# Kernel optimization log

Measured on AMD Instinct MI355X. Metric: run time of the kernel, lower is better.

## Reference

```python
import jax, jax.numpy as jnp
import numpy as np

L, H, D, A, T = 2, 8, 512, 64, 256  # layers, heads, model_dim, attention_dim, target_dim
B, S = 2, 2048
EPS = 1e-5


def _ln(x, g, b):
    m = jnp.mean(x, axis=-1, keepdims=True)
    v = jnp.mean((x - m) ** 2, axis=-1, keepdims=True)
    return (x - m) / jnp.sqrt(v + EPS) * g + b


def setup_inputs() -> dict:
    key = jax.random.key(0)
    ks = jax.random.split(key, 16)
    s = 0.02
    inp = {
        "x": jax.random.normal(ks[0], (B, S, D), jnp.float32),
        # per-head QKV projections, stacked over layers and heads
        "Wq": jax.random.normal(ks[1], (L, H, D, A), jnp.float32) * s,
        "bq": jnp.zeros((L, H, A), jnp.float32),
        "Wk": jax.random.normal(ks[2], (L, H, D, A), jnp.float32) * s,
        "bk": jnp.zeros((L, H, A), jnp.float32),
        "Wv": jax.random.normal(ks[3], (L, H, D, A), jnp.float32) * s,
        "bv": jnp.zeros((L, H, A), jnp.float32),
        # output projection of concatenated heads: [H*A, D]
        "Wo": jax.random.normal(ks[4], (L, H * A, D), jnp.float32) * s,
        "bo": jnp.zeros((L, D), jnp.float32),
        # AddNorm after attention
        "ln1_g": jnp.ones((L, D), jnp.float32),
        "ln1_b": jnp.zeros((L, D), jnp.float32),
        # FFN (hidden_dim == model_dim in this module)
        "W1": jax.random.normal(ks[5], (L, D, D), jnp.float32) * s,
        "b1": jnp.zeros((L, D), jnp.float32),
        "W2": jax.random.normal(ks[6], (L, D, D), jnp.float32) * s,
        "b2": jnp.zeros((L, D), jnp.float32),
        # AddNorm after FFN
        "ln2_g": jnp.ones((L, D), jnp.float32),
        "ln2_b": jnp.zeros((L, D), jnp.float32),
        # final projection to target_dim
        "Wp": jax.random.normal(ks[7], (D, T), jnp.float32) * s,
        "bp": jnp.zeros((T,), jnp.float32),
    }
    return inp


def reference(x, Wq, bq, Wk, bk, Wv, bv, Wo, bo, ln1_g, ln1_b,
              W1, b1, W2, b2, ln2_g, ln2_b, Wp, bp):
    scale = 1.0 / jnp.sqrt(jnp.asarray(A, x.dtype))
    for i in range(L):
        # batched per-head QKV projections (math identical to per-head Linears)
        q = jnp.einsum('bsd,hda->bhsa', x, Wq[i]) + bq[i][:, None, :]
        k = jnp.einsum('bsd,hda->bhsa', x, Wk[i]) + bk[i][:, None, :]
        v = jnp.einsum('bsd,hda->bhsa', x, Wv[i]) + bv[i][:, None, :]
        scores = jnp.einsum('bhsa,bhta->bhst', q, k) * scale  # [B,H,S,S]
        attn = jax.nn.softmax(scores, axis=-1)
        heads = jnp.einsum('bhst,bhta->bhsa', attn, v)        # [B,H,S,A]
        concat = heads.transpose(0, 2, 1, 3).reshape(x.shape[0], x.shape[1], H * A)
        mha = concat @ Wo[i] + bo[i]
        x = _ln(x + mha, ln1_g[i], ln1_b[i])
        ffn = jax.nn.relu(x @ W1[i] + b1[i]) @ W2[i] + b2[i]
        x = _ln(x + ffn, ln2_g[i], ln2_b[i])
    return x @ Wp + bp
```

## Files before the change

kernel.cpp:

```cpp
#include <hip/hip_runtime.h>
#include <hip/hip_bf16.h>

#define MDIM 4096
#define DDIM 512
#define ADIM 64
#define HHEADS 8
#define SLEN 2048
#define TDIM 256
#define SPLIT 4

typedef __attribute__((ext_vector_type(8))) short short8;
typedef __attribute__((ext_vector_type(16))) float f32x16;

__device__ __forceinline__ unsigned short f2bf(float f) {
    union { __hip_bfloat16 h; unsigned short u; } c;
    c.h = __float2bfloat16(f);
    return c.u;
}
__device__ __forceinline__ float bf2f(short s) {
    return __uint_as_float((unsigned)(unsigned short)s << 16);
}

#define N1 524288
#define N2 524288
#define NP 131072
__global__ __launch_bounds__(256) void prep_k(
    const float* __restrict__ Wq, const float* __restrict__ Wk, const float* __restrict__ Wv,
    const float* __restrict__ Wo, const float* __restrict__ W1, const float* __restrict__ W2,
    const float* __restrict__ Wp, const float* __restrict__ x,
    short* __restrict__ Wqt, short* __restrict__ Wkt, short* __restrict__ Wvt,
    short* __restrict__ Wot, short* __restrict__ W1t, short* __restrict__ W2t,
    short* __restrict__ Wpt, short* __restrict__ xbf)
{
    long idx = (long)blockIdx.x * 256 + threadIdx.x;
    if (idx < 3L * N1) {
        int t = (int)(idx / N1);
        int r = (int)(idx % N1);
        int a = r & 63, k = (r >> 6) & 511, hh = r >> 15;
        const float* src = (t == 0) ? Wq : (t == 1) ? Wk : Wv;
        short* dst = (t == 0) ? Wqt : (t == 1) ? Wkt : Wvt;
        dst[((size_t)hh << 15) + (a << 9) + k] = (short)f2bf(src[r]);
        return;
    }
    idx -= 3L * N1;
    if (idx < 3L * N2) {
        int t = (int)(idx / N2);
        int r = (int)(idx % N2);
        int n = r & 511, k = (r >> 9) & 511, i = r >> 18;
        const float* src = (t == 0) ? Wo : (t == 1) ? W1 : W2;
        short* dst = (t == 0) ? Wot : (t == 1) ? W1t : W2t;
        dst[((size_t)i << 18) + (n << 9) + k] = (short)f2bf(src[r]);
        return;
    }
    idx -= 3L * N2;
    if (idx < NP) {
        int r = (int)idx;
        int n = r & 255, k = r >> 8;
        Wpt[n * 512 + k] = (short)f2bf(Wp[r]);
        return;
    }
    idx -= NP;
    xbf[idx] = (short)f2bf(x[idx]);
}

#define LDT 66
__global__ __launch_bounds__(256, 2) void gemm_bf(
    const short* __restrict__ A, const short* __restrict__ Bt,
    const float* __restrict__ bias, void* __restrict__ Cout,
    int M, int N, int K, int flags)
{
    __shared__ short As[64 * LDT];
    __shared__ short Bs[64 * LDT];
    const int tid = threadIdx.x;
    const int wave = tid >> 6, lane = tid & 63;
    const int l31 = lane & 31, hi = lane >> 5;
    const int wm = wave >> 1, wn = wave & 1;
    const int m0 = blockIdx.y * 64, n0 = blockIdx.x * 64;

    f32x16 acc;
#pragma unroll
    for (int r = 0; r < 16; ++r) acc[r] = 0.f;

    const int sr = tid >> 2;
    const int sc = (tid & 3) * 16;

    for (int k0 = 0; k0 < K; k0 += 64) {
        __syncthreads();
        *(short8*)&As[sr * LDT + sc]     = *(const short8*)&A[(size_t)(m0 + sr) * K + k0 + sc];
        *(short8*)&As[sr * LDT + sc + 8] = *(const short8*)&A[(size_t)(m0 + sr) * K + k0 + sc + 8];
        *(short8*)&Bs[sr * LDT + sc]     = *(const short8*)&Bt[(size_t)(n0 + sr) * K + k0 + sc];
        *(short8*)&Bs[sr * LDT + sc + 8] = *(const short8*)&Bt[(size_t)(n0 + sr) * K + k0 + sc + 8];
        __syncthreads();

        short8 af[4], bfm[4];
#pragma unroll
        for (int ks = 0; ks < 4; ++ks) {
            af[ks]  = *(const short8*)&As[(wm * 32 + l31) * LDT + ks * 16 + hi * 8];
            bfm[ks] = *(const short8*)&Bs[(wn * 32 + l31) * LDT + ks * 16 + hi * 8];
        }
#pragma unroll
        for (int ks = 0; ks < 4; ++ks)
            acc = __builtin_amdgcn_mfma_f32_32x32x16_bf16(af[ks], bfm[ks], acc, 0, 0, 0);
    }

    const int col = n0 + wn * 32 + l31;
    const float bb = bias[col];
    const int rbase = m0 + wm * 32 + 4 * hi;
#pragma unroll
    for (int r = 0; r < 16; ++r) {
        int row = rbase + (r & 3) + 8 * (r >> 2);
        float v = acc[r] + bb;
        if (flags & 1) v = fmaxf(v, 0.f);
        if (flags & 2) ((short*)Cout)[(size_t)row * N + col] = (short)f2bf(v);
        else           ((float*)Cout)[(size_t)row * N + col] = v;
    }
}

#define EXPC 0.1803368801111244f

__global__ __launch_bounds__(256, 2) void qkv_bf(
    const short* __restrict__ A,
    const short* __restrict__ Wqt, const short* __restrict__ Wkt, const short* __restrict__ Wvt,
    const float* __restrict__ bq, const float* __restrict__ bk, const float* __restrict__ bv,
    short* __restrict__ Oq, short* __restrict__ Ok, short* __restrict__ Ov)
{
    __shared__ short As[128 * LDT];
    __shared__ short Bs[64 * LDT];
    const int tid = threadIdx.x;
    const int wave = tid >> 6, lane = tid & 63;
    const int l31 = lane & 31, hi = lane >> 5;
    const int wm = wave >> 1, wn = wave & 1;
    const int m0 = blockIdx.y * 128;
    const int nt = blockIdx.x;
    const int which = nt >> 3, h = nt & 7;

    const short* Bt = ((which == 0) ? Wqt : (which == 1) ? Wkt : Wvt) + (size_t)h * 64 * 512;
    const float* bias = ((which == 0) ? bq : (which == 1) ? bk : bv) + h * 64;
    short* Out = (which == 0) ? Oq : (which == 1) ? Ok : Ov;

    f32x16 acc[2];
#pragma unroll
    for (int ms = 0; ms < 2; ++ms)
#pragma unroll
        for (int r = 0; r < 16; ++r) acc[ms][r] = 0.f;

    const int sr = tid >> 3;
    const int sc = (tid & 7) * 8;

    for (int k0 = 0; k0 < 512; k0 += 64) {
        __syncthreads();
#pragma unroll
        for (int p = 0; p < 4; ++p)
            *(short8*)&As[(p * 32 + sr) * LDT + sc] =
                *(const short8*)&A[(size_t)(m0 + p * 32 + sr) * 512 + k0 + sc];
#pragma unroll
        for (int p = 0; p < 2; ++p)
            *(short8*)&Bs[(p * 32 + sr) * LDT + sc] =
                *(const short8*)&Bt[(size_t)(p * 32 + sr) * 512 + k0 + sc];
        __syncthreads();

        short8 af[2][4], bfm[4];
#pragma unroll
        for (int ms = 0; ms < 2; ++ms)
#pragma unroll
            for (int ks = 0; ks < 4; ++ks)
                af[ms][ks] = *(const short8*)&As[(wm * 64 + ms * 32 + l31) * LDT + ks * 16 + hi * 8];
#pragma unroll
        for (int ks = 0; ks < 4; ++ks)
            bfm[ks] = *(const short8*)&Bs[(wn * 32 + l31) * LDT + ks * 16 + hi * 8];
#pragma unroll
        for (int ms = 0; ms < 2; ++ms)
#pragma unroll
            for (int ks = 0; ks < 4; ++ks)
                acc[ms] = __builtin_amdgcn_mfma_f32_32x32x16_bf16(af[ms][ks], bfm[ks], acc[ms], 0, 0, 0);
    }

    const int a = wn * 32 + l31;
    const float bb = bias[a];
    const int b = m0 >> 11;
    const int sb = (m0 & (SLEN - 1)) + wm * 64;
    const int bh = b * HHEADS + h;

    if (which == 0) {
        short* Ob = Out + (size_t)bh * SLEN * 64;
#pragma unroll
        for (int ms = 0; ms < 2; ++ms)
#pragma unroll
            for (int r = 0; r < 16; ++r) {
                int s = sb + ms * 32 + (r & 3) + 8 * (r >> 2) + 4 * hi;
                Ob[(size_t)s * 64 + a] = (short)f2bf((acc[ms][r] + bb) * EXPC);
            }
    } else if (which == 1) {
        short* Ob = Out + (size_t)bh * SLEN * 64;
#pragma unroll
        for (int ms = 0; ms < 2; ++ms)
#pragma unroll
            for (int r = 0; r < 16; ++r) {
                int s = sb + ms * 32 + (r & 3) + 8 * (r >> 2) + 4 * hi;
                Ob[(size_t)s * 64 + a] = (short)f2bf(acc[ms][r] + bb);
            }
    } else {
        short* Ob = Out + ((size_t)bh * 64 + a) * SLEN;
#pragma unroll
        for (int ms = 0; ms < 2; ++ms)
#pragma unroll
            for (int g = 0; g < 4; ++g) {
                int s = sb + ms * 32 + 8 * g + 4 * hi;
                ushort4 w;
                w.x = f2bf(acc[ms][4 * g + 0] + bb);
                w.y = f2bf(acc[ms][4 * g + 1] + bb);
                w.z = f2bf(acc[ms][4 * g + 2] + bb);
                w.w = f2bf(acc[ms][4 * g + 3] + bb);
                *(ushort4*)&Ob[s] = w;
            }
    }
}

__global__ __launch_bounds__(256, 2) void attn_mfma(
    const short* __restrict__ Qb, const short* __restrict__ Kb,
    const short* __restrict__ Vtb, short* __restrict__ Op,
    float* __restrict__ lp)
{
    __shared__ short Ks[64 * 72];
    __shared__ short Vs[64 * 72];

    const int tid = threadIdx.x;
    const int wid = tid >> 6;
    const int lane = tid & 63;
    const int l31 = lane & 31;
    const int hi = lane >> 5;

    const int qt = blockIdx.x;
    const int bh = blockIdx.y;
    const int sp = blockIdx.z;

    const short* Qg = Qb + (size_t)bh * SLEN * 64;
    const short* Kg = Kb + (size_t)bh * SLEN * 64;
    const short* Vg = Vtb + (size_t)bh * 64 * SLEN;

    const int q0 = qt * 256 + wid * 64;

    short8 qf[2][4];
#pragma unroll
    for (int nt = 0; nt < 2; ++nt)
#pragma unroll
        for (int ks = 0; ks < 4; ++ks)
            qf[nt][ks] = *(const short8*)&Qg[(size_t)(q0 + nt * 32 + l31) * 64 + ks * 16 + hi * 8];

    f32x16 oacc[2][2], lacc[2];
#pragma unroll
    for (int nt = 0; nt < 2; ++nt) {
#pragma unroll
        for (int r = 0; r < 16; ++r) lacc[nt][r] = 0.f;
#pragma unroll
        for (int dt = 0; dt < 2; ++dt)
#pragma unroll
            for (int r = 0; r < 16; ++r) oacc[nt][dt][r] = 0.f;
    }

    short8 ones;
#pragma unroll
    for (int j = 0; j < 8; ++j) ones[j] = (short)0x3F80;

    const int srow = tid >> 2;
    const int sch = (tid & 3) * 16;

    for (int kt = 0; kt < 8; ++kt) {
        const int k0 = sp * (SLEN / SPLIT) + kt * 64;
        __syncthreads();
        *(short8*)&Ks[srow * 72 + sch]     = *(const short8*)&Kg[(size_t)(k0 + srow) * 64 + sch];
        *(short8*)&Ks[srow * 72 + sch + 8] = *(const short8*)&Kg[(size_t)(k0 + srow) * 64 + sch + 8];
        *(short8*)&Vs[srow * 72 + sch]     = *(const short8*)&Vg[(size_t)srow * SLEN + k0 + sch];
        *(short8*)&Vs[srow * 72 + sch + 8] = *(const short8*)&Vg[(size_t)srow * SLEN + k0 + sch + 8];
        __syncthreads();

        short8 kf[2][4], vf[2][4];
#pragma unroll
        for (int mt = 0; mt < 2; ++mt)
#pragma unroll
            for (int ks = 0; ks < 4; ++ks)
                kf[mt][ks] = *(const short8*)&Ks[(mt * 32 + l31) * 72 + ks * 16 + hi * 8];
#pragma unroll
        for (int dt = 0; dt < 2; ++dt)
#pragma unroll
            for (int p = 0; p < 4; ++p)
                vf[dt][p] = *(const short8*)&Vs[(dt * 32 + l31) * 72 + p * 16 + hi * 8];

#pragma unroll
        for (int nt = 0; nt < 2; ++nt) {
            f32x16 sacc[2];
#pragma unroll
            for (int mt = 0; mt < 2; ++mt) {
                f32x16 s;
#pragma unroll
                for (int r = 0; r < 16; ++r) s[r] = 0.f;
#pragma unroll
                for (int ks = 0; ks < 4; ++ks)
                    s = __builtin_amdgcn_mfma_f32_32x32x16_bf16(kf[mt][ks], qf[nt][ks], s, 0, 0, 0);
                sacc[mt] = s;
            }

            int2 pk[2][4];
#pragma unroll
            for (int mt = 0; mt < 2; ++mt)
#pragma unroll
                for (int g = 0; g < 4; ++g) {
                    unsigned a0 = __float_as_uint(__builtin_amdgcn_exp2f(sacc[mt][4 * g + 0]));
                    unsigned a1 = __float_as_uint(__builtin_amdgcn_exp2f(sacc[mt][4 * g + 1]));
                    unsigned a2 = __float_as_uint(__builtin_amdgcn_exp2f(sacc[mt][4 * g + 2]));
                    unsigned a3 = __float_as_uint(__builtin_amdgcn_exp2f(sacc[mt][4 * g + 3]));
                    pk[mt][g].x = (int)__builtin_amdgcn_perm(a1, a0, 0x07060302u);
                    pk[mt][g].y = (int)__builtin_amdgcn_perm(a3, a2, 0x07060302u);
                }

            int2 xch[2][2];
#pragma unroll
            for (int mt = 0; mt < 2; ++mt)
#pragma unroll
                for (int h2 = 0; h2 < 2; ++h2) {
                    int2 v = hi ? pk[mt][2 * h2] : pk[mt][2 * h2 + 1];
                    xch[mt][h2].x = __shfl_xor(v.x, 32);
                    xch[mt][h2].y = __shfl_xor(v.y, 32);
                }

#pragma unroll
            for (int p = 0; p < 4; ++p) {
                const int mt = p >> 1, h2 = p & 1;
                const int ga = 2 * h2, gb = 2 * h2 + 1;
                const int2 X = xch[mt][h2];
                union { int4 i; short8 s; } u;
                u.i.x = hi ? X.x : pk[mt][ga].x;
                u.i.y = hi ? X.y : pk[mt][ga].y;
                u.i.z = hi ? pk[mt][gb].x : X.x;
                u.i.w = hi ? pk[mt][gb].y : X.y;
                lacc[nt] = __builtin_amdgcn_mfma_f32_32x32x16_bf16(u.s, ones, lacc[nt], 0, 0, 0);
#pragma unroll
                for (int dt = 0; dt < 2; ++dt)
                    oacc[nt][dt] = __builtin_amdgcn_mfma_f32_32x32x16_bf16(u.s, vf[dt][p], oacc[nt][dt], 0, 0, 0);
            }
        }
    }

#pragma unroll
    for (int nt = 0; nt < 2; ++nt) {
        if (l31 == 0) {
#pragma unroll
            for (int r = 0; r < 16; ++r) {
                int qrow = (r & 3) + 8 * (r >> 2) + 4 * hi;
                lp[((size_t)(sp * 16 + bh)) * SLEN + q0 + nt * 32 + qrow] = lacc[nt][r];
            }
        }
#pragma unroll
        for (int dt = 0; dt < 2; ++dt) {
#pragma unroll
            for (int r = 0; r < 16; ++r) {
                int qrow = (r & 3) + 8 * (r >> 2) + 4 * hi;
                size_t addr = (((size_t)(sp * 16 + bh)) * SLEN + (q0 + nt * 32 + qrow)) * 64 + dt * 32 + l31;
                Op[addr] = (short)f2bf(oacc[nt][dt][r]);
            }
        }
    }
}

__global__ __launch_bounds__(256) void merge_k(
    const short* __restrict__ Op, const float* __restrict__ lp,
    short* __restrict__ hc)
{
    const int g = blockIdx.x * 256 + threadIdx.x;
    const int d4 = g & 15;
    const int s = (g >> 4) & (SLEN - 1);
    const int bh = g >> 15;

    float o[4] = {0.f, 0.f, 0.f, 0.f};
    float ls = 0.f;
#pragma unroll
    for (int sp = 0; sp < SPLIT; ++sp) {
        const size_t base = (((size_t)(sp * 16 + bh)) * SLEN + s);
        ushort4 u4 = *(const ushort4*)&Op[base * 64 + d4 * 4];
        o[0] += bf2f((short)u4.x); o[1] += bf2f((short)u4.y);
        o[2] += bf2f((short)u4.z); o[3] += bf2f((short)u4.w);
        ls += lp[base];
    }
    const int b = bh >> 3, h = bh & 7;
    const float inv = 1.f / ls;
    ushort4 w;
    w.x = f2bf(o[0] * inv); w.y = f2bf(o[1] * inv);
    w.z = f2bf(o[2] * inv); w.w = f2bf(o[3] * inv);
    *(ushort4*)&hc[((size_t)(b * SLEN + s)) * DDIM + h * 64 + d4 * 4] = w;
}

__global__ __launch_bounds__(256) void addnorm_bf(
    short* __restrict__ X, const float* __restrict__ Y,
    const float* __restrict__ g, const float* __restrict__ beta)
{
    const int lane = threadIdx.x & 63;
    const int t = blockIdx.x * 4 + (threadIdx.x >> 6);
    short* xr = X + (size_t)t * DDIM;
    const float* yr = Y + (size_t)t * DDIM;
    const int c0 = lane * 8;

    short8 x8 = *(const short8*)&xr[c0];
    float4 y0 = *(const float4*)&yr[c0];
    float4 y1 = *(const float4*)&yr[c0 + 4];
    float v[8];
    v[0] = bf2f(x8[0]) + y0.x; v[1] = bf2f(x8[1]) + y0.y;
    v[2] = bf2f(x8[2]) + y0.z; v[3] = bf2f(x8[3]) + y0.w;
    v[4] = bf2f(x8[4]) + y1.x; v[5] = bf2f(x8[5]) + y1.y;
    v[6] = bf2f(x8[6]) + y1.z; v[7] = bf2f(x8[7]) + y1.w;

    float s1 = 0.f, s2 = 0.f;
#pragma unroll
    for (int j = 0; j < 8; ++j) { s1 += v[j]; s2 += v[j] * v[j]; }
#pragma unroll
    for (int off = 1; off < 64; off <<= 1) {
        s1 += __shfl_xor(s1, off);
        s2 += __shfl_xor(s2, off);
    }
    float mean = s1 * (1.0f / DDIM);
    float var = s2 * (1.0f / DDIM) - mean * mean;
    float rstd = rsqrtf(var + 1e-5f);

    float4 ga = *(const float4*)&g[c0];
    float4 gb = *(const float4*)&g[c0 + 4];
    float4 ba = *(const float4*)&beta[c0];
    float4 bb = *(const float4*)&beta[c0 + 4];
    float gg[8] = {ga.x, ga.y, ga.z, ga.w, gb.x, gb.y, gb.z, gb.w};
    float bt[8] = {ba.x, ba.y, ba.z, ba.w, bb.x, bb.y, bb.z, bb.w};

    short8 o8;
#pragma unroll
    for (int j = 0; j < 8; ++j)
        o8[j] = (short)f2bf((v[j] - mean) * rstd * gg[j] + bt[j]);
    *(short8*)&xr[c0] = o8;
}

extern "C" void kernel_launch(void* const* d_in, const int* in_sizes, int n_in,
                              void* d_out, int out_size, void* d_ws, size_t ws_size,
                              hipStream_t stream)
{
    (void)in_sizes; (void)n_in; (void)out_size; (void)ws_size;
    const float* x   = (const float*)d_in[0];
    const float* Wq  = (const float*)d_in[1];
    const float* bq  = (const float*)d_in[2];
    const float* Wk  = (const float*)d_in[3];
    const float* bk  = (const float*)d_in[4];
    const float* Wv  = (const float*)d_in[5];
    const float* bv  = (const float*)d_in[6];
    const float* Wo  = (const float*)d_in[7];
    const float* bo  = (const float*)d_in[8];
    const float* g1  = (const float*)d_in[9];
    const float* be1 = (const float*)d_in[10];
    const float* W1  = (const float*)d_in[11];
    const float* b1  = (const float*)d_in[12];
    const float* W2  = (const float*)d_in[13];
    const float* b2  = (const float*)d_in[14];
    const float* g2  = (const float*)d_in[15];
    const float* be2 = (const float*)d_in[16];
    const float* Wp  = (const float*)d_in[17];
    const float* bp  = (const float*)d_in[18];

    char* wsb = (char*)d_ws;
    const size_t MB = 1024 * 1024;
    short* xbf   = (short*)(wsb + 0);
    short* Qbuf  = (short*)(wsb + 4 * MB);
    short* Kbuf  = (short*)(wsb + 8 * MB);
    short* Vtbuf = (short*)(wsb + 12 * MB);
    short* Opart = (short*)(wsb + 16 * MB);
    float* y     = (float*)(wsb + 16 * MB);
    short* hidbf = (short*)(wsb + 24 * MB);
    float* lpart = (float*)(wsb + 32 * MB);
    short* hcbf  = Qbuf;
    short* Wqt   = (short*)(wsb + 33 * MB);
    short* Wkt   = (short*)(wsb + 34 * MB);
    short* Wvt   = (short*)(wsb + 35 * MB);
    short* Wot   = (short*)(wsb + 36 * MB);
    short* W1t   = (short*)(wsb + 37 * MB);
    short* W2t   = (short*)(wsb + 38 * MB);
    short* Wpt   = (short*)(wsb + 39 * MB);

    prep_k<<<20992, 256, 0, stream>>>(Wq, Wk, Wv, Wo, W1, W2, Wp, x,
                                      Wqt, Wkt, Wvt, Wot, W1t, W2t, Wpt, xbf);

    for (int i = 0; i < 2; ++i) {
        const size_t wOffQ = (size_t)i * 262144;
        const size_t wOffS = (size_t)i * 262144;
        qkv_bf<<<dim3(24, 32), 256, 0, stream>>>(
            xbf, Wqt + wOffQ, Wkt + wOffQ, Wvt + wOffQ,
            bq + i * 512, bk + i * 512, bv + i * 512,
            Qbuf, Kbuf, Vtbuf);
        attn_mfma<<<dim3(8, 16, SPLIT), 256, 0, stream>>>(Qbuf, Kbuf, Vtbuf, Opart, lpart);
        merge_k<<<2048, 256, 0, stream>>>(Opart, lpart, hcbf);
        gemm_bf<<<dim3(8, 64), 256, 0, stream>>>(
            hcbf, Wot + wOffS, bo + i * 512, y, MDIM, DDIM, DDIM, 0);
        addnorm_bf<<<1024, 256, 0, stream>>>(xbf, y, g1 + i * 512, be1 + i * 512);
        gemm_bf<<<dim3(8, 64), 256, 0, stream>>>(
            xbf, W1t + wOffS, b1 + i * 512, hidbf, MDIM, DDIM, DDIM, 3);
        gemm_bf<<<dim3(8, 64), 256, 0, stream>>>(
            hidbf, W2t + wOffS, b2 + i * 512, y, MDIM, DDIM, DDIM, 0);
        addnorm_bf<<<1024, 256, 0, stream>>>(xbf, y, g2 + i * 512, be2 + i * 512);
    }
    gemm_bf<<<dim3(4, 64), 256, 0, stream>>>(
        xbf, Wpt, bp, (float*)d_out, MDIM, TDIM, DDIM, 0);
}
```

Before: 293.7 us.

## Prefetch K/V tiles into registers, compute softmax row sums with VALU, add MFMA priority

The attention kernel now loads the next K/V tile from global memory into registers while the current tile is being computed, which overlaps global latency with MFMA work. The row-sum of exponentials is now accumulated with scalar adds on bf16-truncated values and reduced with one lane shuffle, replacing the extra MFMA against a ones vector per step. s_setprio is raised around the MFMA blocks so waves issuing matrix work get scheduling priority. The changes cost extra registers for the prefetch and add VALU work for the sums.

Result: no change. 297.5 us (+1.3%).

```diff
diff --git a/kernel.cpp b/kernel.cpp
--- a/kernel.cpp
+++ b/kernel.cpp
@@ -247,32 +247,39 @@
         for (int ks = 0; ks < 4; ++ks)
             qf[nt][ks] = *(const short8*)&Qg[(size_t)(q0 + nt * 32 + l31) * 64 + ks * 16 + hi * 8];
 
-    f32x16 oacc[2][2], lacc[2];
-#pragma unroll
-    for (int nt = 0; nt < 2; ++nt) {
-#pragma unroll
-        for (int r = 0; r < 16; ++r) lacc[nt][r] = 0.f;
+    f32x16 oacc[2][2];
+    float lsum[2] = {0.f, 0.f};
+#pragma unroll
+    for (int nt = 0; nt < 2; ++nt)
 #pragma unroll
         for (int dt = 0; dt < 2; ++dt)
 #pragma unroll
             for (int r = 0; r < 16; ++r) oacc[nt][dt][r] = 0.f;
-    }
-
-    short8 ones;
-#pragma unroll
-    for (int j = 0; j < 8; ++j) ones[j] = (short)0x3F80;
 
     const int srow = tid >> 2;
     const int sch = (tid & 3) * 16;
+    const int kbase = sp * (SLEN / SPLIT);
+
+    short8 rk0 = *(const short8*)&Kg[(size_t)(kbase + srow) * 64 + sch];
+    short8 rk1 = *(const short8*)&Kg[(size_t)(kbase + srow) * 64 + sch + 8];
+    short8 rv0 = *(const short8*)&Vg[(size_t)srow * SLEN + kbase + sch];
+    short8 rv1 = *(const short8*)&Vg[(size_t)srow * SLEN + kbase + sch + 8];
 
     for (int kt = 0; kt < 8; ++kt) {
-        const int k0 = sp * (SLEN / SPLIT) + kt * 64;
         __syncthreads();
-        *(short8*)&Ks[srow * 72 + sch]     = *(const short8*)&Kg[(size_t)(k0 + srow) * 64 + sch];
-        *(short8*)&Ks[srow * 72 + sch + 8] = *(const short8*)&Kg[(size_t)(k0 + srow) * 64 + sch + 8];
-        *(short8*)&Vs[srow * 72 + sch]     = *(const short8*)&Vg[(size_t)srow * SLEN + k0 + sch];
-        *(short8*)&Vs[srow * 72 + sch + 8] = *(const short8*)&Vg[(size_t)srow * SLEN + k0 + sch + 8];
+        *(short8*)&Ks[srow * 72 + sch]     = rk0;
+        *(short8*)&Ks[srow * 72 + sch + 8] = rk1;
+        *(short8*)&Vs[srow * 72 + sch]     = rv0;
+        *(short8*)&Vs[srow * 72 + sch + 8] = rv1;
         __syncthreads();
+
+        if (kt < 7) {
+            const int k0n = kbase + (kt + 1) * 64;
+            rk0 = *(const short8*)&Kg[(size_t)(k0n + srow) * 64 + sch];
+            rk1 = *(const short8*)&Kg[(size_t)(k0n + srow) * 64 + sch + 8];
+            rv0 = *(const short8*)&Vg[(size_t)srow * SLEN + k0n + sch];
+            rv1 = *(const short8*)&Vg[(size_t)srow * SLEN + k0n + sch + 8];
+        }
 
         short8 kf[2][4], vf[2][4];
 #pragma unroll
@@ -289,6 +296,7 @@
 #pragma unroll
         for (int nt = 0; nt < 2; ++nt) {
             f32x16 sacc[2];
+            __builtin_amdgcn_s_setprio(1);
 #pragma unroll
             for (int mt = 0; mt < 2; ++mt) {
                 f32x16 s;
@@ -299,6 +307,7 @@
                     s = __builtin_amdgcn_mfma_f32_32x32x16_bf16(kf[mt][ks], qf[nt][ks], s, 0, 0, 0);
                 sacc[mt] = s;
             }
+            __builtin_amdgcn_s_setprio(0);
 
             int2 pk[2][4];
 #pragma unroll
@@ -309,6 +318,11 @@
                     unsigned a1 = __float_as_uint(__builtin_amdgcn_exp2f(sacc[mt][4 * g + 1]));
                     unsigned a2 = __float_as_uint(__builtin_amdgcn_exp2f(sacc[mt][4 * g + 2]));
                     unsigned a3 = __float_as_uint(__builtin_amdgcn_exp2f(sacc[mt][4 * g + 3]));
+                    float t0 = __uint_as_float(a0 & 0xffff0000u);
+                    float t1 = __uint_as_float(a1 & 0xffff0000u);
+                    float t2 = __uint_as_float(a2 & 0xffff0000u);
+                    float t3 = __uint_as_float(a3 & 0xffff0000u);
+                    lsum[nt] += (t0 + t1) + (t2 + t3);
                     pk[mt][g].x = (int)__builtin_amdgcn_perm(a1, a0, 0x07060302u);
                     pk[mt][g].y = (int)__builtin_amdgcn_perm(a3, a2, 0x07060302u);
                 }
@@ -323,6 +337,7 @@
                     xch[mt][h2].y = __shfl_xor(v.y, 32);
                 }
 
+            __builtin_amdgcn_s_setprio(1);
 #pragma unroll
             for (int p = 0; p < 4; ++p) {
                 const int mt = p >> 1, h2 = p & 1;
@@ -333,23 +348,19 @@
                 u.i.y = hi ? X.y : pk[mt][ga].y;
                 u.i.z = hi ? pk[mt][gb].x : X.x;
                 u.i.w = hi ? pk[mt][gb].y : X.y;
-                lacc[nt] = __builtin_amdgcn_mfma_f32_32x32x16_bf16(u.s, ones, lacc[nt], 0, 0, 0);
 #pragma unroll
                 for (int dt = 0; dt < 2; ++dt)
                     oacc[nt][dt] = __builtin_amdgcn_mfma_f32_32x32x16_bf16(u.s, vf[dt][p], oacc[nt][dt], 0, 0, 0);
             }
+            __builtin_amdgcn_s_setprio(0);
         }
     }
 
 #pragma unroll
     for (int nt = 0; nt < 2; ++nt) {
-        if (l31 == 0) {
-#pragma unroll
-            for (int r = 0; r < 16; ++r) {
-                int qrow = (r & 3) + 8 * (r >> 2) + 4 * hi;
-                lp[((size_t)(sp * 16 + bh)) * SLEN + q0 + nt * 32 + qrow] = lacc[nt][r];
-            }
-        }
+        float lt = lsum[nt] + __shfl_xor(lsum[nt], 32);
+        if (hi == 0)
+            lp[((size_t)(sp * 16 + bh)) * SLEN + q0 + nt * 32 + l31] = lt;
 #pragma unroll
         for (int dt = 0; dt < 2; ++dt) {
 #pragma unroll
```
